# Kernel optimization log

Hardware: AMD Instinct MI355X
Metric: run time of the kernel (lower is better)

## Reference

```python
import jax, jax.numpy as jnp
import numpy as np

def setup_inputs() -> dict:
    key = jax.random.key(0)
    k1, k2 = jax.random.split(key)
    B, T, C = 32, 1024, 384
    x = jax.random.normal(k1, (B, T, C), dtype=jnp.float32)
    duration = jax.random.randint(k2, (B, T), 0, 8, dtype=jnp.int64)
    return {"x": x, "duration": duration, "max_mel_len": 4096}


def reference(x, duration, max_mel_len):
    # Equivalent to the original per-batch expand-matrix matmul:
    # out[b, m] = x[b, t] where t is the token whose duration-interval covers
    # frame m; frames beyond sum(duration[b]) are zero.
    B, T, C = x.shape
    cs = jnp.cumsum(duration, axis=1)                      # [B, T] end offsets
    total = cs[:, -1]                                      # [B] expanded lengths
    frames = jnp.arange(max_mel_len)                       # [M]
    # token index for each output frame: first t with cs[b, t] > m
    tok = jax.vmap(lambda c: jnp.searchsorted(c, frames, side="right"))(cs)  # [B, M]
    tok = jnp.clip(tok, 0, T - 1)
    out = jnp.take_along_axis(x, tok[:, :, None], axis=1)  # [B, M, C]
    valid = frames[None, :] < total[:, None]               # [B, M]
    out = jnp.where(valid[:, :, None], out, jnp.zeros((), dtype=x.dtype))
    return out, total
```

## Files before the change

### kernel.cpp

```cpp
#include <hip/hip_runtime.h>

#define BB 32
#define TT 1024
#define CC 384
#define MAXMEL 4096

__global__ __launch_bounds__(TT) void lr_scan_kernel(const int* __restrict__ dur,
                                                     int* __restrict__ cs,
                                                     float* __restrict__ out_total) {
    __shared__ int s[TT];
    const int b = blockIdx.x;
    const int tid = threadIdx.x;
    s[tid] = dur[b * TT + tid];
    __syncthreads();
    #pragma unroll
    for (int off = 1; off < TT; off <<= 1) {
        int v = (tid >= off) ? s[tid - off] : 0;
        __syncthreads();
        s[tid] += v;
        __syncthreads();
    }
    cs[b * TT + tid] = s[tid];
    if (tid == TT - 1) out_total[b] = (float)s[tid];
}

__global__ __launch_bounds__(256) void lr_expand_kernel(const float* __restrict__ x,
                                                        const int* __restrict__ cs,
                                                        float* __restrict__ out) {
    __shared__ int s_cs[TT];
    const int b = blockIdx.y;
    const int chunk = blockIdx.x;
    const int tid = threadIdx.x;

    for (int j = tid; j < TT; j += 256) s_cs[j] = cs[b * TT + j];
    __syncthreads();

    const int total = s_cs[TT - 1];
    const int fsub = tid >> 5;
    const int lane = tid & 31;
    const int frame = chunk * 8 + fsub;

    float4* outp = (float4*)(out + ((size_t)b * MAXMEL + frame) * CC);

    if (frame < total) {
        int lo = 0, hi = TT;
        while (lo < hi) {
            int mid = (lo + hi) >> 1;
            if (s_cs[mid] <= frame) lo = mid + 1; else hi = mid;
        }
        const int tok = min(lo, TT - 1);
        const float4* src = (const float4*)(x + ((size_t)b * TT + tok) * CC);
        #pragma unroll
        for (int k = 0; k < 3; ++k) outp[lane + k * 32] = src[lane + k * 32];
    } else {
        const float4 z = make_float4(0.f, 0.f, 0.f, 0.f);
        #pragma unroll
        for (int k = 0; k < 3; ++k) outp[lane + k * 32] = z;
    }
}

extern "C" void kernel_launch(void* const* d_in, const int* in_sizes, int n_in,
                              void* d_out, int out_size, void* d_ws, size_t ws_size,
                              hipStream_t stream) {
    const float* x = (const float*)d_in[0];
    const int* dur = (const int*)d_in[1];
    float* out = (float*)d_out;
    int* cs = (int*)d_ws;
    float* out_total = out + (size_t)BB * MAXMEL * CC;

    lr_scan_kernel<<<BB, TT, 0, stream>>>(dur, cs, out_total);
    lr_expand_kernel<<<dim3(MAXMEL / 8, BB), 256, 0, stream>>>(x, cs, out);
}
```

Baseline: 244.6 us.

## Precompute per-frame token indices in scan kernel; use wave-shuffle scan

The scan kernel now uses a wave-level shuffle scan instead of a shared-memory Hillis-Steele loop. It also does the binary search for every output frame once and writes 16-bit token indices, with a sentinel marking frames to zero. The expand kernel then does one 2-byte load per frame instead of staging the cumsum in shared memory and searching. This takes the search and shared-memory staging out of the bandwidth-bound copy kernel, at the cost of a serial 32-block search kernel and an extra workspace buffer. A fallback path with larger copy blocks is used when the workspace is too small.

```diff
diff --git a/kernel.cpp b/kernel.cpp
--- a/kernel.cpp
+++ b/kernel.cpp
@@ -1,55 +1,74 @@
 #include <hip/hip_runtime.h>
+#include <stdint.h>
 
 #define BB 32
 #define TT 1024
 #define CC 384
 #define MAXMEL 4096
 
-__global__ __launch_bounds__(TT) void lr_scan_kernel(const int* __restrict__ dur,
-                                                     int* __restrict__ cs,
-                                                     float* __restrict__ out_total) {
-    __shared__ int s[TT];
+__device__ __forceinline__ int block_scan_1024(const int* __restrict__ dur, int b,
+                                               int* s_cs) {
+    __shared__ int s_wsum[16];
+    const int tid = threadIdx.x;
+    const int lane = tid & 63;
+    const int wid = tid >> 6;
+    int v = dur[b * TT + tid];
+    #pragma unroll
+    for (int off = 1; off < 64; off <<= 1) {
+        int n = __shfl_up(v, off, 64);
+        if (lane >= off) v += n;
+    }
+    if (lane == 63) s_wsum[wid] = v;
+    __syncthreads();
+    if (wid == 0 && lane < 16) {
+        int w = s_wsum[lane];
+        #pragma unroll
+        for (int off = 1; off < 16; off <<= 1) {
+            int n = __shfl_up(w, off, 64);
+            if (lane >= off) w += n;
+        }
+        s_wsum[lane] = w;
+    }
+    __syncthreads();
+    if (wid > 0) v += s_wsum[wid - 1];
+    s_cs[tid] = v;
+    __syncthreads();
+    return s_cs[TT - 1];
+}
+
+
+__global__ __launch_bounds__(1024) void lr_scan_tok16(const int* __restrict__ dur,
+                                                      uint16_t* __restrict__ tok,
+                                                      float* __restrict__ out_total) {
+    __shared__ int s_cs[TT];
     const int b = blockIdx.x;
     const int tid = threadIdx.x;
-    s[tid] = dur[b * TT + tid];
-    __syncthreads();
-    #pragma unroll
-    for (int off = 1; off < TT; off <<= 1) {
-        int v = (tid >= off) ? s[tid - off] : 0;
-        __syncthreads();
-        s[tid] += v;
-        __syncthreads();
+    const int total = block_scan_1024(dur, b, s_cs);
+    if (tid == 0) out_total[b] = (float)total;
+    for (int f = tid; f < MAXMEL; f += 1024) {
+        uint16_t t = 0xFFFFu;
+        if (f < total) {
+            int lo = 0, hi = TT;
+            while (lo < hi) {
+                int mid = (lo + hi) >> 1;
+                if (s_cs[mid] <= f) lo = mid + 1; else hi = mid;
+            }
+            t = (uint16_t)min(lo, TT - 1);
+        }
+        tok[b * MAXMEL + f] = t;
     }
-    cs[b * TT + tid] = s[tid];
-    if (tid == TT - 1) out_total[b] = (float)s[tid];
 }
 
-__global__ __launch_bounds__(256) void lr_expand_kernel(const float* __restrict__ x,
-                                                        const int* __restrict__ cs,
-                                                        float* __restrict__ out) {
-    __shared__ int s_cs[TT];
+__global__ __launch_bounds__(256) void lr_expand_tok16(const float* __restrict__ x,
+                                                       const uint16_t* __restrict__ tok,
+                                                       float* __restrict__ out) {
     const int b = blockIdx.y;
-    const int chunk = blockIdx.x;
-    const int tid = threadIdx.x;
-
-    for (int j = tid; j < TT; j += 256) s_cs[j] = cs[b * TT + j];
-    __syncthreads();
-
-    const int total = s_cs[TT - 1];
-    const int fsub = tid >> 5;
-    const int lane = tid & 31;
-    const int frame = chunk * 8 + fsub;
-
+    const int frame = blockIdx.x * 8 + (threadIdx.x >> 5);
+    const int lane = threadIdx.x & 31;
+    const uint32_t t = tok[b * MAXMEL + frame];
     float4* outp = (float4*)(out + ((size_t)b * MAXMEL + frame) * CC);
-
-    if (frame < total) {
-        int lo = 0, hi = TT;
-        while (lo < hi) {
-            int mid = (lo + hi) >> 1;
-            if (s_cs[mid] <= frame) lo = mid + 1; else hi = mid;
-        }
-        const int tok = min(lo, TT - 1);
-        const float4* src = (const float4*)(x + ((size_t)b * TT + tok) * CC);
+    if (t != 0xFFFFu) {
+        const float4* src = (const float4*)(x + ((size_t)b * TT + t) * CC);
         #pragma unroll
         for (int k = 0; k < 3; ++k) outp[lane + k * 32] = src[lane + k * 32];
     } else {
@@ -59,15 +78,62 @@
     }
 }
 
+
+__global__ __launch_bounds__(1024) void lr_scan_cs(const int* __restrict__ dur,
+                                                   int* __restrict__ cs,
+                                                   float* __restrict__ out_total) {
+    __shared__ int s_cs[TT];
+    const int b = blockIdx.x;
+    const int tid = threadIdx.x;
+    const int total = block_scan_1024(dur, b, s_cs);
+    cs[b * TT + tid] = s_cs[tid];
+    if (tid == 0) out_total[b] = (float)total;
+}
+
+__global__ __launch_bounds__(1024) void lr_expand_search(const float* __restrict__ x,
+                                                         const int* __restrict__ cs,
+                                                         float* __restrict__ out) {
+    __shared__ int s_cs[TT];
+    const int b = blockIdx.y;
+    const int tid = threadIdx.x;
+    s_cs[tid] = cs[b * TT + tid];
+    __syncthreads();
+    const int total = s_cs[TT - 1];
+    const int frame = blockIdx.x * 64 + (tid >> 4);
+    const int lane = tid & 15;
+    float4* outp = (float4*)(out + ((size_t)b * MAXMEL + frame) * CC);
+    if (frame < total) {
+        int lo = 0, hi = TT;
+        while (lo < hi) {
+            int mid = (lo + hi) >> 1;
+            if (s_cs[mid] <= frame) lo = mid + 1; else hi = mid;
+        }
+        const int t = min(lo, TT - 1);
+        const float4* src = (const float4*)(x + ((size_t)b * TT + t) * CC);
+        #pragma unroll
+        for (int k = 0; k < 6; ++k) outp[lane + k * 16] = src[lane + k * 16];
+    } else {
+        const float4 z = make_float4(0.f, 0.f, 0.f, 0.f);
+        #pragma unroll
+        for (int k = 0; k < 6; ++k) outp[lane + k * 16] = z;
+    }
+}
+
 extern "C" void kernel_launch(void* const* d_in, const int* in_sizes, int n_in,
                               void* d_out, int out_size, void* d_ws, size_t ws_size,
                               hipStream_t stream) {
     const float* x = (const float*)d_in[0];
     const int* dur = (const int*)d_in[1];
     float* out = (float*)d_out;
-    int* cs = (int*)d_ws;
     float* out_total = out + (size_t)BB * MAXMEL * CC;
 
-    lr_scan_kernel<<<BB, TT, 0, stream>>>(dur, cs, out_total);
-    lr_expand_kernel<<<dim3(MAXMEL / 8, BB), 256, 0, stream>>>(x, cs, out);
+    if (ws_size >= (size_t)BB * MAXMEL * sizeof(uint16_t)) {
+        uint16_t* tok = (uint16_t*)d_ws;
+        lr_scan_tok16<<<BB, 1024, 0, stream>>>(dur, tok, out_total);
+        lr_expand_tok16<<<dim3(MAXMEL / 8, BB), 256, 0, stream>>>(x, tok, out);
+    } else {
+        int* cs = (int*)d_ws;
+        lr_scan_cs<<<BB, 1024, 0, stream>>>(dur, cs, out_total);
+        lr_expand_search<<<dim3(MAXMEL / 64, BB), 1024, 0, stream>>>(x, cs, out);
+    }
 }
```

Result: no change. 244.6 us (-0.0%).

## Fuse duration scan into expand kernel with wave-shuffle prefix sum

Applied to the files above, without the earlier changes.

Merges the separate cumsum kernel and the expand kernel into one launch. Each block recomputes the per-batch prefix sum from durations using wave-level shuffles plus a small cross-wave pass, which removes the workspace round trip and the second launch. Blocks now cover 32 frames with 512 threads, and output writes use nontemporal stores to avoid cache pollution. The cost is that the scan is recomputed redundantly in every block.

```diff
diff --git a/kernel.cpp b/kernel.cpp
--- a/kernel.cpp
+++ b/kernel.cpp
@@ -1,61 +1,77 @@
 #include <hip/hip_runtime.h>
+#include <stdint.h>
 
 #define BB 32
 #define TT 1024
 #define CC 384
 #define MAXMEL 4096
 
-__global__ __launch_bounds__(TT) void lr_scan_kernel(const int* __restrict__ dur,
-                                                     int* __restrict__ cs,
-                                                     float* __restrict__ out_total) {
-    __shared__ int s[TT];
-    const int b = blockIdx.x;
+typedef float f4 __attribute__((ext_vector_type(4)));
+
+__global__ __launch_bounds__(512) void lr_fused(const float* __restrict__ x,
+                                                const int* __restrict__ dur,
+                                                float* __restrict__ out,
+                                                float* __restrict__ out_total) {
+    __shared__ int s_cs[TT];
+    __shared__ int s_wsum[8];
+    const int b = blockIdx.y;
     const int tid = threadIdx.x;
-    s[tid] = dur[b * TT + tid];
+    const int lane64 = tid & 63;
+    const int wid = tid >> 6;
+
+    const int2 d = ((const int2*)(dur + b * TT))[tid];
+    const int pair = d.x + d.y;
+    int inc = pair;
+    #pragma unroll
+    for (int off = 1; off < 64; off <<= 1) {
+        int n = __shfl_up(inc, off, 64);
+        if (lane64 >= off) inc += n;
+    }
+    if (lane64 == 63) s_wsum[wid] = inc;
     __syncthreads();
-    #pragma unroll
-    for (int off = 1; off < TT; off <<= 1) {
-        int v = (tid >= off) ? s[tid - off] : 0;
-        __syncthreads();
-        s[tid] += v;
-        __syncthreads();
+    if (wid == 0 && lane64 < 8) {
+        int w = s_wsum[lane64];
+        #pragma unroll
+        for (int off = 1; off < 8; off <<= 1) {
+            int n = __shfl_up(w, off, 64);
+            if (lane64 >= off) w += n;
+        }
+        s_wsum[lane64] = w;
     }
-    cs[b * TT + tid] = s[tid];
-    if (tid == TT - 1) out_total[b] = (float)s[tid];
-}
-
-__global__ __launch_bounds__(256) void lr_expand_kernel(const float* __restrict__ x,
-                                                        const int* __restrict__ cs,
-                                                        float* __restrict__ out) {
-    __shared__ int s_cs[TT];
-    const int b = blockIdx.y;
-    const int chunk = blockIdx.x;
-    const int tid = threadIdx.x;
-
-    for (int j = tid; j < TT; j += 256) s_cs[j] = cs[b * TT + j];
+    __syncthreads();
+    int excl = inc - pair + (wid > 0 ? s_wsum[wid - 1] : 0);
+    s_cs[2 * tid]     = excl + d.x;
+    s_cs[2 * tid + 1] = excl + pair;
     __syncthreads();
 
     const int total = s_cs[TT - 1];
+    if (blockIdx.x == 0 && tid == 0) out_total[b] = (float)total;
+
+    const int lane32 = tid & 31;
     const int fsub = tid >> 5;
-    const int lane = tid & 31;
-    const int frame = chunk * 8 + fsub;
-
-    float4* outp = (float4*)(out + ((size_t)b * MAXMEL + frame) * CC);
-
-    if (frame < total) {
-        int lo = 0, hi = TT;
-        while (lo < hi) {
-            int mid = (lo + hi) >> 1;
-            if (s_cs[mid] <= frame) lo = mid + 1; else hi = mid;
+    #pragma unroll
+    for (int g = 0; g < 2; ++g) {
+        const int frame = blockIdx.x * 32 + g * 16 + fsub;
+        f4* outp = (f4*)(out + ((size_t)b * MAXMEL + frame) * CC);
+        if (frame < total) {
+            int lo = 0, hi = TT;
+            while (lo < hi) {
+                int mid = (lo + hi) >> 1;
+                if (s_cs[mid] <= frame) lo = mid + 1; else hi = mid;
+            }
+            const int t = min(lo, TT - 1);
+            const f4* src = (const f4*)(x + ((size_t)b * TT + t) * CC);
+            #pragma unroll
+            for (int k = 0; k < 3; ++k) {
+                f4 v = src[lane32 + k * 32];
+                __builtin_nontemporal_store(v, &outp[lane32 + k * 32]);
+            }
+        } else {
+            const f4 z = {0.f, 0.f, 0.f, 0.f};
+            #pragma unroll
+            for (int k = 0; k < 3; ++k)
+                __builtin_nontemporal_store(z, &outp[lane32 + k * 32]);
         }
-        const int tok = min(lo, TT - 1);
-        const float4* src = (const float4*)(x + ((size_t)b * TT + tok) * CC);
-        #pragma unroll
-        for (int k = 0; k < 3; ++k) outp[lane + k * 32] = src[lane + k * 32];
-    } else {
-        const float4 z = make_float4(0.f, 0.f, 0.f, 0.f);
-        #pragma unroll
-        for (int k = 0; k < 3; ++k) outp[lane + k * 32] = z;
     }
 }
 
@@ -65,9 +81,6 @@
     const float* x = (const float*)d_in[0];
     const int* dur = (const int*)d_in[1];
     float* out = (float*)d_out;
-    int* cs = (int*)d_ws;
     float* out_total = out + (size_t)BB * MAXMEL * CC;
-
-    lr_scan_kernel<<<BB, TT, 0, stream>>>(dur, cs, out_total);
-    lr_expand_kernel<<<dim3(MAXMEL / 8, BB), 256, 0, stream>>>(x, cs, out);
+    lr_fused<<<dim3(MAXMEL / 32, BB), 512, 0, stream>>>(x, dur, out, out_total);
 }
```

After: 240.6 us. About the same (-1.6%).
